# Optimization experiments

Hardware: AMD Instinct MI355X
Metric: run time of the kernel (lower is better)

Reference implementation:

```python
import jax, jax.numpy as jnp
import numpy as np

H_G, W_G = 9, 25
N_NODES = H_G * W_G  # 225


def _grid_edge_index():
    # 8-connected grid graph INCLUDING self loops (di=dj=0), matching build_grid_edge_index.
    # PyG GATConv's remove_self_loops+add_self_loops leaves this edge set unchanged.
    edges = []
    for i in range(H_G):
        for j in range(W_G):
            nid = i * W_G + j
            for di in (-1, 0, 1):
                for dj in (-1, 0, 1):
                    ni, nj = i + di, j + dj
                    if 0 <= ni < H_G and 0 <= nj < W_G:
                        edges.append((nid, ni * W_G + nj))
    return jnp.asarray(np.array(edges, dtype=np.int32).T)  # [2, 1825]


def _gat(x, edge_index, W, a_src, a_dst, bias, concat):
    # x: [B, N, F_in]; W: [F_in, heads*d]; a_src/a_dst: [heads, d]
    B = x.shape[0]
    heads, d = a_src.shape
    h = (x @ W).reshape(B, N_NODES, heads, d)          # [B,N,H,D]
    src, dst = edge_index[0], edge_index[1]            # message flows src -> dst
    asrc = jnp.einsum('bnhd,hd->bnh', h, a_src)        # [B,N,H]
    adst = jnp.einsum('bnhd,hd->bnh', h, a_dst)
    e = jax.nn.leaky_relu(asrc[:, src] + adst[:, dst], 0.2)  # [B,E,H]
    et = jnp.transpose(e, (1, 0, 2))                   # [E,B,H] (segment ops over leading axis)
    m = jax.ops.segment_max(et, dst, num_segments=N_NODES)  # [N,B,H]
    ex = jnp.exp(et - m[dst])
    s = jax.ops.segment_sum(ex, dst, num_segments=N_NODES)
    alpha = ex / s[dst]                                # softmax over incoming edges per node
    ht = jnp.transpose(h, (1, 0, 2, 3))                # [N,B,H,D]
    out = jax.ops.segment_sum(alpha[..., None] * ht[src], dst, num_segments=N_NODES)  # [N,B,H,D]
    out = jnp.transpose(out, (1, 0, 2, 3))             # [B,N,H,D]
    if concat:
        out = out.reshape(B, N_NODES, heads * d)
    else:
        out = out.mean(axis=2)
    return out + bias


def setup_inputs() -> dict:
    key = jax.random.key(0)
    ks = jax.random.split(key, 16)
    B = 128
    s = 0.02
    inp = {
        'x4': jax.random.normal(ks[0], (B, 2048, 9, 25), dtype=jnp.float32),
        'pool_w': jax.random.normal(ks[1], (8, 2048), dtype=jnp.float32) * s,
        'pool_b': jnp.zeros((8,), dtype=jnp.float32),
        'gat1_w': jax.random.normal(ks[2], (8, 64), dtype=jnp.float32) * s,
        'gat1_asrc': jax.random.normal(ks[3], (4, 16), dtype=jnp.float32) * s,
        'gat1_adst': jax.random.normal(ks[4], (4, 16), dtype=jnp.float32) * s,
        'gat1_b': jnp.zeros((64,), dtype=jnp.float32),
        'gat2_w': jax.random.normal(ks[5], (64, 8), dtype=jnp.float32) * s,
        'gat2_asrc': jax.random.normal(ks[6], (1, 8), dtype=jnp.float32) * s,
        'gat2_adst': jax.random.normal(ks[7], (1, 8), dtype=jnp.float32) * s,
        'gat2_b': jnp.zeros((8,), dtype=jnp.float32),
        'w1': jax.random.normal(ks[8], (1800, 2048), dtype=jnp.float32) * 0.01,
        'b1': jnp.zeros((2048,), dtype=jnp.float32),
        'w2': jax.random.normal(ks[9], (2048, 20800), dtype=jnp.float32) * 0.01,
        'b2': jnp.zeros((20800,), dtype=jnp.float32),
        'edge_index': _grid_edge_index(),
    }
    return inp


def reference(x4, pool_w, pool_b, gat1_w, gat1_asrc, gat1_adst, gat1_b,
              gat2_w, gat2_asrc, gat2_adst, gat2_b, w1, b1, w2, b2, edge_index):
    B = x4.shape[0]
    # 1x1 conv pool: 2048 -> 8 channels (already 9x25, adaptive_avg_pool2d is identity)
    fea = jnp.einsum('bchw,oc->bohw', x4, pool_w) + pool_b[None, :, None, None]
    fea = fea.reshape(B, 8, N_NODES).transpose(0, 2, 1)  # [B, 225, 8]
    x1 = jax.nn.relu(_gat(fea, edge_index, gat1_w, gat1_asrc, gat1_adst, gat1_b, concat=True))
    x2 = _gat(x1, edge_index, gat2_w, gat2_asrc, gat2_adst, gat2_b, concat=False)  # [B,225,8]
    flat = x2.reshape(B, -1)                             # [B, 1800]
    hid = jax.nn.relu(flat @ w1 + b1)
    out = hid @ w2 + b2
    return out.reshape(-1, 100, 52, 4)
```

## Files before the change

kernel.cpp:

```cpp
#include <hip/hip_runtime.h>
#include <hip/hip_bf16.h>


typedef __attribute__((ext_vector_type(8))) short bh8_t;
typedef __attribute__((ext_vector_type(4))) float f32x4;

static __device__ __forceinline__ short f2bs(float f) {
    __hip_bfloat16 h = __float2bfloat16(f);
    return *reinterpret_cast<short*>(&h);
}
static __device__ __forceinline__ unsigned pack2(short a, short b) {
    return (unsigned)(unsigned short)a | ((unsigned)(unsigned short)b << 16);
}

__global__ __launch_bounds__(256) void pool_kernel(const float* __restrict__ x4,
                                                   const float* __restrict__ pool_w,
                                                   float* __restrict__ part) {
    const int b  = blockIdx.x >> 3;
    const int ch = blockIdx.x & 7;
    __shared__ __align__(16) float ws[256 * 8];
    const int tid = threadIdx.x;
    for (int i = tid; i < 2048; i += 256)
        ws[i] = pool_w[(i & 7) * 2048 + ch * 256 + (i >> 3)];
    __syncthreads();
    if (tid < 225) {
        const float* xp = x4 + ((size_t)b * 2048 + (size_t)ch * 256) * 225 + tid;
        float a0 = 0, a1 = 0, a2 = 0, a3 = 0, a4 = 0, a5 = 0, a6 = 0, a7 = 0;
#pragma unroll 8
        for (int c = 0; c < 256; ++c) {
            float v = xp[c * 225];
            const float4 wa = *reinterpret_cast<const float4*>(&ws[c * 8]);
            const float4 wb = *reinterpret_cast<const float4*>(&ws[c * 8 + 4]);
            a0 += v * wa.x; a1 += v * wa.y; a2 += v * wa.z; a3 += v * wa.w;
            a4 += v * wb.x; a5 += v * wb.y; a6 += v * wb.z; a7 += v * wb.w;
        }
        float* dst = part + (size_t)b * 14400 + ch * 1800 + tid * 8;
        dst[0] = a0; dst[1] = a1; dst[2] = a2; dst[3] = a3;
        dst[4] = a4; dst[5] = a5; dst[6] = a6; dst[7] = a7;
    }
}

__global__ __launch_bounds__(256) void gat1_kernel(const float* __restrict__ part,
                                                   const float* __restrict__ pool_b,
                                                   const float* __restrict__ w,
                                                   const float* __restrict__ a_src,
                                                   const float* __restrict__ a_dst,
                                                   const float* __restrict__ bias,
                                                   float* __restrict__ x1) {
    __shared__ __align__(16) float fea[1800];
    __shared__ __align__(16) float h[14400];
    const int b = blockIdx.x;
    const int tid = threadIdx.x;

    for (int i = tid; i < 1800; i += 256) {
        const float* p = part + (size_t)b * 14400 + i;
        float s = 0;
#pragma unroll
        for (int c = 0; c < 8; ++c) s += p[c * 1800];
        fea[i] = s + pool_b[i & 7];
    }
    __syncthreads();

    {
        const int o = tid & 63, mr = tid >> 6;
        float wv[8];
#pragma unroll
        for (int k = 0; k < 8; ++k) wv[k] = w[k * 64 + o];
        for (int n = mr; n < 225; n += 4) {
            float acc = 0;
#pragma unroll
            for (int k = 0; k < 8; ++k) acc += fea[n * 8 + k] * wv[k];
            h[n * 64 + o] = acc;
        }
    }
    __syncthreads();

    for (int t = tid; t < 900; t += 256) {
        const int n = t >> 2, hd = t & 3;
        const float* hp = &h[n * 64 + hd * 16];
        float as = 0, ad = 0;
#pragma unroll
        for (int d = 0; d < 16; ++d) {
            float hv = hp[d];
            as += hv * a_src[hd * 16 + d];
            ad += hv * a_dst[hd * 16 + d];
        }
        fea[t] = as;
        fea[900 + t] = ad;
    }
    __syncthreads();

    for (int task = tid; task < 900; task += 256) {
        const int n = task >> 2, hd = task & 3;
        const int i = n / 25, j = n % 25;
        const float adn = fea[900 + task];
        float e[9];
        int sid[9];
        float mx = -1e30f;
#pragma unroll
        for (int t9 = 0; t9 < 9; ++t9) {
            const int di = t9 / 3 - 1, dj = t9 % 3 - 1;
            const int ni = i + di, nj = j + dj;
            const bool valid = ((unsigned)ni < 9u) && ((unsigned)nj < 25u);
            const int s = valid ? ni * 25 + nj : n;
            sid[t9] = s;
            float ev = fea[s * 4 + hd] + adn;
            ev = ev >= 0.f ? ev : 0.2f * ev;
            e[t9] = valid ? ev : -1e30f;
            mx = fmaxf(mx, e[t9]);
        }
        float sum = 0;
#pragma unroll
        for (int t9 = 0; t9 < 9; ++t9) {
            float ex = __expf(e[t9] - mx);
            e[t9] = ex;
            sum += ex;
        }
        const float inv = 1.f / sum;
        float out[16] = {};
#pragma unroll
        for (int t9 = 0; t9 < 9; ++t9) {
            const float al = e[t9] * inv;
            const float* hp = &h[sid[t9] * 64 + hd * 16];
#pragma unroll
            for (int d = 0; d < 16; ++d) out[d] += al * hp[d];
        }
        float* dst = x1 + (size_t)b * 14400 + n * 64 + hd * 16;
        const float* bp = bias + hd * 16;
#pragma unroll
        for (int d = 0; d < 16; ++d) dst[d] = fmaxf(out[d] + bp[d], 0.f);
    }
}

__global__ __launch_bounds__(256) void gat2_kernel(const float* __restrict__ x1,
                                                   const float* __restrict__ w,
                                                   const float* __restrict__ a_src,
                                                   const float* __restrict__ a_dst,
                                                   const float* __restrict__ bias,
                                                   short* __restrict__ flat) {
    __shared__ __align__(16) float xs[14400];
    __shared__ __align__(16) float h[1800];
    const int b = blockIdx.x;
    const int tid = threadIdx.x;
    for (int i = tid; i < 14400; i += 256) xs[i] = x1[(size_t)b * 14400 + i];
    __syncthreads();
    for (int t = tid; t < 1800; t += 256) {
        const int o = t & 7, n = t >> 3;
        float acc = 0;
#pragma unroll 8
        for (int k = 0; k < 64; ++k) acc += xs[n * 64 + k] * w[k * 8 + o];
        h[t] = acc;
    }
    __syncthreads();
    if (tid < 225) {
        const int n = tid, i = n / 25, j = n % 25;
        float av[8], dv[8];
#pragma unroll
        for (int d = 0; d < 8; ++d) { av[d] = a_src[d]; dv[d] = a_dst[d]; }
        float adn = 0;
#pragma unroll
        for (int d = 0; d < 8; ++d) adn += h[n * 8 + d] * dv[d];
        float e[9];
        int sid[9];
        float mx = -1e30f;
#pragma unroll
        for (int t9 = 0; t9 < 9; ++t9) {
            const int di = t9 / 3 - 1, dj = t9 % 3 - 1;
            const int ni = i + di, nj = j + dj;
            const bool valid = ((unsigned)ni < 9u) && ((unsigned)nj < 25u);
            const int s = valid ? ni * 25 + nj : n;
            sid[t9] = s;
            float as = 0;
#pragma unroll
            for (int d = 0; d < 8; ++d) as += h[s * 8 + d] * av[d];
            float ev = as + adn;
            ev = ev >= 0.f ? ev : 0.2f * ev;
            e[t9] = valid ? ev : -1e30f;
            mx = fmaxf(mx, e[t9]);
        }
        float sum = 0;
#pragma unroll
        for (int t9 = 0; t9 < 9; ++t9) {
            float ex = __expf(e[t9] - mx);
            e[t9] = ex;
            sum += ex;
        }
        const float inv = 1.f / sum;
        float out[8] = {};
#pragma unroll
        for (int t9 = 0; t9 < 9; ++t9) {
            const float al = e[t9] * inv;
            const float* hp = &h[sid[t9] * 8];
#pragma unroll
            for (int d = 0; d < 8; ++d) out[d] += al * hp[d];
        }
        short* dst = flat + (size_t)b * 1800 + n * 8;
#pragma unroll
        for (int d = 0; d < 8; ++d) dst[d] = f2bs(out[d] + bias[d]);
    }
}

template <int BN, int MT, int NT, int NWN, bool RELU, bool OUT_BF16>
__global__ __launch_bounds__(256) void gemm_mfma(const short* __restrict__ A,
                                                 const float* __restrict__ Wf,
                                                 const float* __restrict__ bias,
                                                 void* __restrict__ outp,
                                                 int K, int N) {
    constexpr int LDT = 40;
    __shared__ __align__(16) short sA[128 * LDT];
    __shared__ __align__(16) short sB[BN * LDT];
    const int tid = threadIdx.x;
    const int lane = tid & 63;
    const int wave = tid >> 6;
    const int n0 = blockIdx.x * BN;
    const int wm0 = (wave / NWN) * (MT * 16);
    const int wn0 = (wave % NWN) * (NT * 16);
    const int lm = lane & 15;
    const int lkb = (lane >> 4) * 8;

    const int am = tid >> 1;
    const int akh = tid & 1;
    constexpr int EPT = (32 * BN) / 256;
    const int bn_ = tid % BN;
    const int bk0 = (tid / BN) * EPT;

    f32x4 acc[MT][NT] = {};

    const int nkt = (K + 31) >> 5;
    for (int kt = 0; kt < nkt; ++kt) {
        const int k0 = kt << 5;
        if (k0 + 32 <= K) {
            const uint4* src = reinterpret_cast<const uint4*>(A + (size_t)am * K + k0 + akh * 16);
            uint4 v0 = src[0];
            uint4 v1 = src[1];
            float bv[EPT];
#pragma unroll
            for (int jj = 0; jj < EPT; ++jj)
                bv[jj] = Wf[(size_t)(k0 + bk0 + jj) * N + n0 + bn_];
            uint4* dstA = reinterpret_cast<uint4*>(&sA[am * LDT + akh * 16]);
            dstA[0] = v0;
            dstA[1] = v1;
            unsigned uw[EPT / 2];
#pragma unroll
            for (int jj = 0; jj < EPT / 2; ++jj)
                uw[jj] = pack2(f2bs(bv[2 * jj]), f2bs(bv[2 * jj + 1]));
            if constexpr (EPT == 8) {
                uint4 u;
                u.x = uw[0]; u.y = uw[1]; u.z = uw[2]; u.w = uw[3];
                *reinterpret_cast<uint4*>(&sB[bn_ * LDT + bk0]) = u;
            } else {
                *reinterpret_cast<unsigned*>(&sB[bn_ * LDT + bk0]) = uw[0];
            }
        } else {
#pragma unroll
            for (int jj = 0; jj < 16; ++jj) {
                const int kk = k0 + akh * 16 + jj;
                sA[am * LDT + akh * 16 + jj] = (kk < K) ? A[(size_t)am * K + kk] : (short)0;
            }
#pragma unroll
            for (int jj = 0; jj < EPT; ++jj) {
                const int kk = k0 + bk0 + jj;
                const float v = (kk < K) ? Wf[(size_t)kk * N + n0 + bn_] : 0.f;
                sB[bn_ * LDT + bk0 + jj] = f2bs(v);
            }
        }
        __syncthreads();
        bh8_t bfr[NT];
#pragma unroll
        for (int nt = 0; nt < NT; ++nt)
            bfr[nt] = *reinterpret_cast<const bh8_t*>(&sB[(wn0 + nt * 16 + lm) * LDT + lkb]);
#pragma unroll
        for (int mt = 0; mt < MT; ++mt) {
            bh8_t afr = *reinterpret_cast<const bh8_t*>(&sA[(wm0 + mt * 16 + lm) * LDT + lkb]);
#pragma unroll
            for (int nt = 0; nt < NT; ++nt)
                acc[mt][nt] = __builtin_amdgcn_mfma_f32_16x16x32_bf16(afr, bfr[nt], acc[mt][nt], 0, 0, 0);
        }
        __syncthreads();
    }
    const int rg = lane >> 4;
#pragma unroll
    for (int nt = 0; nt < NT; ++nt) {
        const int n = n0 + wn0 + nt * 16 + lm;
        const float bv = bias[n];
#pragma unroll
        for (int mt = 0; mt < MT; ++mt) {
#pragma unroll
            for (int r = 0; r < 4; ++r) {
                const int m = wm0 + mt * 16 + rg * 4 + r;
                float v = acc[mt][nt][r] + bv;
                if (RELU) v = fmaxf(v, 0.f);
                if (OUT_BF16)
                    reinterpret_cast<short*>(outp)[(size_t)m * N + n] = f2bs(v);
                else
                    reinterpret_cast<float*>(outp)[(size_t)m * N + n] = v;
            }
        }
    }
}

extern "C" void kernel_launch(void* const* d_in, const int* in_sizes, int n_in,
                              void* d_out, int out_size, void* d_ws, size_t ws_size,
                              hipStream_t stream) {
    const float* x4        = (const float*)d_in[0];
    const float* pool_w    = (const float*)d_in[1];
    const float* pool_b    = (const float*)d_in[2];
    const float* gat1_w    = (const float*)d_in[3];
    const float* gat1_asrc = (const float*)d_in[4];
    const float* gat1_adst = (const float*)d_in[5];
    const float* gat1_b    = (const float*)d_in[6];
    const float* gat2_w    = (const float*)d_in[7];
    const float* gat2_asrc = (const float*)d_in[8];
    const float* gat2_adst = (const float*)d_in[9];
    const float* gat2_b    = (const float*)d_in[10];
    const float* w1        = (const float*)d_in[11];
    const float* b1        = (const float*)d_in[12];
    const float* w2        = (const float*)d_in[13];
    const float* b2        = (const float*)d_in[14];
    float* out = (float*)d_out;

    char* ws = (char*)d_ws;
    float* part = (float*)ws;
    float* x1   = (float*)(ws + 7372800);
    short* flat = (short*)(ws + 14745600);
    short* hid  = (short*)(ws + 15206400);

    pool_kernel<<<1024, 256, 0, stream>>>(x4, pool_w, part);
    gat1_kernel<<<128, 256, 0, stream>>>(part, pool_b, gat1_w, gat1_asrc, gat1_adst, gat1_b, x1);
    gat2_kernel<<<128, 256, 0, stream>>>(x1, gat2_w, gat2_asrc, gat2_adst, gat2_b, flat);
    gemm_mfma<16, 2, 1, 1, true, true><<<128, 256, 0, stream>>>(flat, w1, b1, (void*)hid, 1800, 2048);
    gemm_mfma<64, 4, 2, 2, false, false><<<325, 256, 0, stream>>>(hid, w2, b2, (void*)out, 2048, 20800);
}
```

Before: 569.5 us.

## Fuse GAT layers, double-buffer GEMM tiles, pad K, simplify pool kernel

Merges the two GAT kernels into one per-batch kernel that keeps layer-1 output in shared memory, so x1 no longer round-trips through global memory. The MFMA GEMM now uses double-buffered shared tiles with register prefetch of the next K tile, and the flat activations are zero-padded to K=1824 so the ragged-tail branch goes away. The pool kernel reads weights straight from global/cache instead of staging them in LDS. Risks include extra register pressure from the o1[4][16] array and uncoalesced weight loads in the pool kernel.

Result: faster. 546.8 us (-4.0%).

```diff
diff --git a/kernel.cpp b/kernel.cpp
--- a/kernel.cpp
+++ b/kernel.cpp
@@ -18,36 +18,34 @@
                                                    float* __restrict__ part) {
     const int b  = blockIdx.x >> 3;
     const int ch = blockIdx.x & 7;
-    __shared__ __align__(16) float ws[256 * 8];
     const int tid = threadIdx.x;
-    for (int i = tid; i < 2048; i += 256)
-        ws[i] = pool_w[(i & 7) * 2048 + ch * 256 + (i >> 3)];
-    __syncthreads();
-    if (tid < 225) {
-        const float* xp = x4 + ((size_t)b * 2048 + (size_t)ch * 256) * 225 + tid;
-        float a0 = 0, a1 = 0, a2 = 0, a3 = 0, a4 = 0, a5 = 0, a6 = 0, a7 = 0;
+    if (tid >= 225) return;
+    const float* xp = x4 + ((size_t)b * 2048 + (size_t)ch * 256) * 225 + tid;
+    const float* wp = pool_w + ch * 256;
+    float a[8] = {};
 #pragma unroll 8
-        for (int c = 0; c < 256; ++c) {
-            float v = xp[c * 225];
-            const float4 wa = *reinterpret_cast<const float4*>(&ws[c * 8]);
-            const float4 wb = *reinterpret_cast<const float4*>(&ws[c * 8 + 4]);
-            a0 += v * wa.x; a1 += v * wa.y; a2 += v * wa.z; a3 += v * wa.w;
-            a4 += v * wb.x; a5 += v * wb.y; a6 += v * wb.z; a7 += v * wb.w;
-        }
-        float* dst = part + (size_t)b * 14400 + ch * 1800 + tid * 8;
-        dst[0] = a0; dst[1] = a1; dst[2] = a2; dst[3] = a3;
-        dst[4] = a4; dst[5] = a5; dst[6] = a6; dst[7] = a7;
-    }
-}
-
-__global__ __launch_bounds__(256) void gat1_kernel(const float* __restrict__ part,
-                                                   const float* __restrict__ pool_b,
-                                                   const float* __restrict__ w,
-                                                   const float* __restrict__ a_src,
-                                                   const float* __restrict__ a_dst,
-                                                   const float* __restrict__ bias,
-                                                   float* __restrict__ x1) {
-    __shared__ __align__(16) float fea[1800];
+    for (int c = 0; c < 256; ++c) {
+        const float v = xp[c * 225];
+#pragma unroll
+        for (int o = 0; o < 8; ++o) a[o] += v * wp[o * 2048 + c];
+    }
+    float* dst = part + (size_t)b * 14400 + ch * 1800 + tid * 8;
+    *reinterpret_cast<float4*>(dst)     = make_float4(a[0], a[1], a[2], a[3]);
+    *reinterpret_cast<float4*>(dst + 4) = make_float4(a[4], a[5], a[6], a[7]);
+}
+
+__global__ __launch_bounds__(256) void gat_kernel(const float* __restrict__ part,
+                                                  const float* __restrict__ pool_b,
+                                                  const float* __restrict__ w1g,
+                                                  const float* __restrict__ a1src,
+                                                  const float* __restrict__ a1dst,
+                                                  const float* __restrict__ b1g,
+                                                  const float* __restrict__ w2g,
+                                                  const float* __restrict__ a2src,
+                                                  const float* __restrict__ a2dst,
+                                                  const float* __restrict__ b2g,
+                                                  short* __restrict__ flat) {
+    __shared__ __align__(16) float att[1800];
     __shared__ __align__(16) float h[14400];
     const int b = blockIdx.x;
     const int tid = threadIdx.x;
@@ -57,7 +55,7 @@
         float s = 0;
 #pragma unroll
         for (int c = 0; c < 8; ++c) s += p[c * 1800];
-        fea[i] = s + pool_b[i & 7];
+        att[i] = s + pool_b[i & 7];
     }
     __syncthreads();
 
@@ -65,11 +63,11 @@
         const int o = tid & 63, mr = tid >> 6;
         float wv[8];
 #pragma unroll
-        for (int k = 0; k < 8; ++k) wv[k] = w[k * 64 + o];
+        for (int k = 0; k < 8; ++k) wv[k] = w1g[k * 64 + o];
         for (int n = mr; n < 225; n += 4) {
             float acc = 0;
 #pragma unroll
-            for (int k = 0; k < 8; ++k) acc += fea[n * 8 + k] * wv[k];
+            for (int k = 0; k < 8; ++k) acc += att[n * 8 + k] * wv[k];
             h[n * 64 + o] = acc;
         }
     }
@@ -82,84 +80,96 @@
 #pragma unroll
         for (int d = 0; d < 16; ++d) {
             float hv = hp[d];
-            as += hv * a_src[hd * 16 + d];
-            ad += hv * a_dst[hd * 16 + d];
-        }
-        fea[t] = as;
-        fea[900 + t] = ad;
-    }
-    __syncthreads();
-
-    for (int task = tid; task < 900; task += 256) {
-        const int n = task >> 2, hd = task & 3;
-        const int i = n / 25, j = n % 25;
-        const float adn = fea[900 + task];
-        float e[9];
-        int sid[9];
-        float mx = -1e30f;
-#pragma unroll
-        for (int t9 = 0; t9 < 9; ++t9) {
-            const int di = t9 / 3 - 1, dj = t9 % 3 - 1;
-            const int ni = i + di, nj = j + dj;
-            const bool valid = ((unsigned)ni < 9u) && ((unsigned)nj < 25u);
-            const int s = valid ? ni * 25 + nj : n;
-            sid[t9] = s;
-            float ev = fea[s * 4 + hd] + adn;
-            ev = ev >= 0.f ? ev : 0.2f * ev;
-            e[t9] = valid ? ev : -1e30f;
-            mx = fmaxf(mx, e[t9]);
-        }
-        float sum = 0;
-#pragma unroll
-        for (int t9 = 0; t9 < 9; ++t9) {
-            float ex = __expf(e[t9] - mx);
-            e[t9] = ex;
-            sum += ex;
-        }
-        const float inv = 1.f / sum;
-        float out[16] = {};
-#pragma unroll
-        for (int t9 = 0; t9 < 9; ++t9) {
-            const float al = e[t9] * inv;
-            const float* hp = &h[sid[t9] * 64 + hd * 16];
-#pragma unroll
-            for (int d = 0; d < 16; ++d) out[d] += al * hp[d];
-        }
-        float* dst = x1 + (size_t)b * 14400 + n * 64 + hd * 16;
-        const float* bp = bias + hd * 16;
-#pragma unroll
-        for (int d = 0; d < 16; ++d) dst[d] = fmaxf(out[d] + bp[d], 0.f);
-    }
-}
-
-__global__ __launch_bounds__(256) void gat2_kernel(const float* __restrict__ x1,
-                                                   const float* __restrict__ w,
-                                                   const float* __restrict__ a_src,
-                                                   const float* __restrict__ a_dst,
-                                                   const float* __restrict__ bias,
-                                                   short* __restrict__ flat) {
-    __shared__ __align__(16) float xs[14400];
-    __shared__ __align__(16) float h[1800];
-    const int b = blockIdx.x;
-    const int tid = threadIdx.x;
-    for (int i = tid; i < 14400; i += 256) xs[i] = x1[(size_t)b * 14400 + i];
-    __syncthreads();
-    for (int t = tid; t < 1800; t += 256) {
-        const int o = t & 7, n = t >> 3;
-        float acc = 0;
-#pragma unroll 8
-        for (int k = 0; k < 64; ++k) acc += xs[n * 64 + k] * w[k * 8 + o];
-        h[t] = acc;
-    }
-    __syncthreads();
+            as += hv * a1src[hd * 16 + d];
+            ad += hv * a1dst[hd * 16 + d];
+        }
+        att[t] = as;
+        att[900 + t] = ad;
+    }
+    __syncthreads();
+
+    float o1[4][16];
+#pragma unroll
+    for (int r = 0; r < 4; ++r) {
+        const int task = tid + 256 * r;
+        if (task < 900) {
+            const int n = task >> 2, hd = task & 3;
+            const int i = n / 25, j = n % 25;
+            const float adn = att[900 + task];
+            float e[9];
+            int sid[9];
+            float mx = -1e30f;
+#pragma unroll
+            for (int t9 = 0; t9 < 9; ++t9) {
+                const int di = t9 / 3 - 1, dj = t9 % 3 - 1;
+                const int ni = i + di, nj = j + dj;
+                const bool valid = ((unsigned)ni < 9u) && ((unsigned)nj < 25u);
+                const int s = valid ? ni * 25 + nj : n;
+                sid[t9] = s;
+                float ev = att[s * 4 + hd] + adn;
+                ev = ev >= 0.f ? ev : 0.2f * ev;
+                e[t9] = valid ? ev : -1e30f;
+                mx = fmaxf(mx, e[t9]);
+            }
+            float sum = 0;
+#pragma unroll
+            for (int t9 = 0; t9 < 9; ++t9) {
+                float ex = __expf(e[t9] - mx);
+                e[t9] = ex;
+                sum += ex;
+            }
+            const float inv = 1.f / sum;
+            float out[16] = {};
+#pragma unroll
+            for (int t9 = 0; t9 < 9; ++t9) {
+                const float al = e[t9] * inv;
+                const float* hp = &h[sid[t9] * 64 + hd * 16];
+#pragma unroll
+                for (int d = 0; d < 16; ++d) out[d] += al * hp[d];
+            }
+            const float* bp = b1g + hd * 16;
+#pragma unroll
+            for (int d = 0; d < 16; ++d) o1[r][d] = fmaxf(out[d] + bp[d], 0.f);
+        }
+    }
+    __syncthreads();
+
+#pragma unroll
+    for (int r = 0; r < 4; ++r) {
+        const int task = tid + 256 * r;
+        if (task < 900) {
+            const int n = task >> 2, hd = task & 3;
+#pragma unroll
+            for (int d = 0; d < 16; ++d) h[n * 64 + hd * 16 + d] = o1[r][d];
+        }
+    }
+    __syncthreads();
+
+    if (tid < 225) {
+        const int n = tid;
+        float acc8[8] = {};
+#pragma unroll 4
+        for (int k = 0; k < 64; k += 4) {
+            const float4 xv = *reinterpret_cast<const float4*>(&h[n * 64 + k]);
+#pragma unroll
+            for (int o = 0; o < 8; ++o) {
+                acc8[o] += xv.x * w2g[k * 8 + o] + xv.y * w2g[(k + 1) * 8 + o]
+                         + xv.z * w2g[(k + 2) * 8 + o] + xv.w * w2g[(k + 3) * 8 + o];
+            }
+        }
+#pragma unroll
+        for (int o = 0; o < 8; ++o) att[n * 8 + o] = acc8[o];
+    }
+    __syncthreads();
+
     if (tid < 225) {
         const int n = tid, i = n / 25, j = n % 25;
         float av[8], dv[8];
 #pragma unroll
-        for (int d = 0; d < 8; ++d) { av[d] = a_src[d]; dv[d] = a_dst[d]; }
+        for (int d = 0; d < 8; ++d) { av[d] = a2src[d]; dv[d] = a2dst[d]; }
         float adn = 0;
 #pragma unroll
-        for (int d = 0; d < 8; ++d) adn += h[n * 8 + d] * dv[d];
+        for (int d = 0; d < 8; ++d) adn += att[n * 8 + d] * dv[d];
         float e[9];
         int sid[9];
         float mx = -1e30f;
@@ -172,7 +182,7 @@
             sid[t9] = s;
             float as = 0;
 #pragma unroll
-            for (int d = 0; d < 8; ++d) as += h[s * 8 + d] * av[d];
+            for (int d = 0; d < 8; ++d) as += att[s * 8 + d] * av[d];
             float ev = as + adn;
             ev = ev >= 0.f ? ev : 0.2f * ev;
             e[t9] = valid ? ev : -1e30f;
@@ -190,14 +200,15 @@
 #pragma unroll
         for (int t9 = 0; t9 < 9; ++t9) {
             const float al = e[t9] * inv;
-            const float* hp = &h[sid[t9] * 8];
+            const float* hp = &att[sid[t9] * 8];
 #pragma unroll
             for (int d = 0; d < 8; ++d) out[d] += al * hp[d];
         }
-        short* dst = flat + (size_t)b * 1800 + n * 8;
-#pragma unroll
-        for (int d = 0; d < 8; ++d) dst[d] = f2bs(out[d] + bias[d]);
-    }
+        short* dst = flat + (size_t)b * 1824 + n * 8;
+#pragma unroll
+        for (int d = 0; d < 8; ++d) dst[d] = f2bs(out[d] + b2g[d]);
+    }
+    if (tid < 24) flat[(size_t)b * 1824 + 1800 + tid] = 0;
 }
 
 template <int BN, int MT, int NT, int NWN, bool RELU, bool OUT_BF16>
@@ -205,10 +216,10 @@
                                                  const float* __restrict__ Wf,
                                                  const float* __restrict__ bias,
                                                  void* __restrict__ outp,
-                                                 int K, int N) {
+                                                 int K, int Kw, int N) {
     constexpr int LDT = 40;
-    __shared__ __align__(16) short sA[128 * LDT];
-    __shared__ __align__(16) short sB[BN * LDT];
+    __shared__ __align__(16) short sA[2][128 * LDT];
+    __shared__ __align__(16) short sB[2][BN * LDT];
     const int tid = threadIdx.x;
     const int lane = tid & 63;
     const int wave = tid >> 6;
@@ -225,70 +236,75 @@
     const int bk0 = (tid / BN) * EPT;
 
     f32x4 acc[MT][NT] = {};
-
-    const int nkt = (K + 31) >> 5;
+    const int nkt = K >> 5;
+
+    uint4 va0, va1;
+    float bv[EPT];
+
+    auto LOAD = [&](int kt) {
+        const int k0 = kt << 5;
+        const uint4* src = reinterpret_cast<const uint4*>(A + (size_t)am * K + k0 + akh * 16);
+        va0 = src[0];
+        va1 = src[1];
+#pragma unroll
+        for (int jj = 0; jj < EPT; ++jj) {
+            int kk = k0 + bk0 + jj;
+            if (kk >= Kw) kk = Kw - 1;
+            bv[jj] = Wf[(size_t)kk * N + n0 + bn_];
+        }
+    };
+    auto STORE = [&](int buf) {
+        uint4* dstA = reinterpret_cast<uint4*>(&sA[buf][am * LDT + akh * 16]);
+        dstA[0] = va0;
+        dstA[1] = va1;
+        unsigned uw[EPT / 2];
+#pragma unroll
+        for (int jj = 0; jj < EPT / 2; ++jj)
+            uw[jj] = pack2(f2bs(bv[2 * jj]), f2bs(bv[2 * jj + 1]));
+        if constexpr (EPT == 8) {
+            uint4 u;
+            u.x = uw[0]; u.y = uw[1]; u.z = uw[2]; u.w = uw[3];
+            *reinterpret_cast<uint4*>(&sB[buf][bn_ * LDT + bk0]) = u;
+        } else {
+            *reinterpret_cast<unsigned*>(&sB[buf][bn_ * LDT + bk0]) = uw[0];
+        }
+    };
+
+    LOAD(0);
+    STORE(0);
+    __syncthreads();
+
+    int cur = 0;
     for (int kt = 0; kt < nkt; ++kt) {
-        const int k0 = kt << 5;
-        if (k0 + 32 <= K) {
-            const uint4* src = reinterpret_cast<const uint4*>(A + (size_t)am * K + k0 + akh * 16);
-            uint4 v0 = src[0];
-            uint4 v1 = src[1];
-            float bv[EPT];
-#pragma unroll
-            for (int jj = 0; jj < EPT; ++jj)
-                bv[jj] = Wf[(size_t)(k0 + bk0 + jj) * N + n0 + bn_];
-            uint4* dstA = reinterpret_cast<uint4*>(&sA[am * LDT + akh * 16]);
-            dstA[0] = v0;
-            dstA[1] = v1;
-            unsigned uw[EPT / 2];
-#pragma unroll
-            for (int jj = 0; jj < EPT / 2; ++jj)
-                uw[jj] = pack2(f2bs(bv[2 * jj]), f2bs(bv[2 * jj + 1]));
-            if constexpr (EPT == 8) {
-                uint4 u;
-                u.x = uw[0]; u.y = uw[1]; u.z = uw[2]; u.w = uw[3];
-                *reinterpret_cast<uint4*>(&sB[bn_ * LDT + bk0]) = u;
-            } else {
-                *reinterpret_cast<unsigned*>(&sB[bn_ * LDT + bk0]) = uw[0];
-            }
-        } else {
-#pragma unroll
-            for (int jj = 0; jj < 16; ++jj) {
-                const int kk = k0 + akh * 16 + jj;
-                sA[am * LDT + akh * 16 + jj] = (kk < K) ? A[(size_t)am * K + kk] : (short)0;
-            }
-#pragma unroll
-            for (int jj = 0; jj < EPT; ++jj) {
-                const int kk = k0 + bk0 + jj;
-                const float v = (kk < K) ? Wf[(size_t)kk * N + n0 + bn_] : 0.f;
-                sB[bn_ * LDT + bk0 + jj] = f2bs(v);
-            }
-        }
-        __syncthreads();
+        const bool more = (kt + 1 < nkt);
+        if (more) LOAD(kt + 1);
         bh8_t bfr[NT];
 #pragma unroll
         for (int nt = 0; nt < NT; ++nt)
-            bfr[nt] = *reinterpret_cast<const bh8_t*>(&sB[(wn0 + nt * 16 + lm) * LDT + lkb]);
+            bfr[nt] = *reinterpret_cast<const bh8_t*>(&sB[cur][(wn0 + nt * 16 + lm) * LDT + lkb]);
 #pragma unroll
         for (int mt = 0; mt < MT; ++mt) {
-            bh8_t afr = *reinterpret_cast<const bh8_t*>(&sA[(wm0 + mt * 16 + lm) * LDT + lkb]);
+            bh8_t afr = *reinterpret_cast<const bh8_t*>(&sA[cur][(wm0 + mt * 16 + lm) * LDT + lkb]);
 #pragma unroll
             for (int nt = 0; nt < NT; ++nt)
                 acc[mt][nt] = __builtin_amdgcn_mfma_f32_16x16x32_bf16(afr, bfr[nt], acc[mt][nt], 0, 0, 0);
         }
+        if (more) STORE(cur ^ 1);
         __syncthreads();
-    }
+        cur ^= 1;
+    }
+
     const int rg = lane >> 4;
 #pragma unroll
     for (int nt = 0; nt < NT; ++nt) {
         const int n = n0 + wn0 + nt * 16 + lm;
-        const float bv = bias[n];
+        const float bvv = bias[n];
 #pragma unroll
         for (int mt = 0; mt < MT; ++mt) {
 #pragma unroll
             for (int r = 0; r < 4; ++r) {
                 const int m = wm0 + mt * 16 + rg * 4 + r;
-                float v = acc[mt][nt][r] + bv;
+                float v = acc[mt][nt][r] + bvv;
                 if (RELU) v = fmaxf(v, 0.f);
                 if (OUT_BF16)
                     reinterpret_cast<short*>(outp)[(size_t)m * N + n] = f2bs(v);
@@ -321,13 +337,12 @@
 
     char* ws = (char*)d_ws;
     float* part = (float*)ws;
-    float* x1   = (float*)(ws + 7372800);
-    short* flat = (short*)(ws + 14745600);
-    short* hid  = (short*)(ws + 15206400);
+    short* flat = (short*)(ws + 7372800);
+    short* hid  = (short*)(ws + 7372800 + 466944);
 
     pool_kernel<<<1024, 256, 0, stream>>>(x4, pool_w, part);
-    gat1_kernel<<<128, 256, 0, stream>>>(part, pool_b, gat1_w, gat1_asrc, gat1_adst, gat1_b, x1);
-    gat2_kernel<<<128, 256, 0, stream>>>(x1, gat2_w, gat2_asrc, gat2_adst, gat2_b, flat);
-    gemm_mfma<16, 2, 1, 1, true, true><<<128, 256, 0, stream>>>(flat, w1, b1, (void*)hid, 1800, 2048);
-    gemm_mfma<64, 4, 2, 2, false, false><<<325, 256, 0, stream>>>(hid, w2, b2, (void*)out, 2048, 20800);
-}
+    gat_kernel<<<128, 256, 0, stream>>>(part, pool_b, gat1_w, gat1_asrc, gat1_adst, gat1_b,
+                                        gat2_w, gat2_asrc, gat2_adst, gat2_b, flat);
+    gemm_mfma<16, 2, 1, 1, true, true><<<128, 256, 0, stream>>>(flat, w1, b1, (void*)hid, 1824, 1800, 2048);
+    gemm_mfma<64, 4, 2, 2, false, false><<<325, 256, 0, stream>>>(hid, w2, b2, (void*)out, 2048, 2048, 20800);
+}
```
